# Performance work log

Measured on AMD Instinct MI355X. Metric: run time of the kernel, lower is better.

## Reference

```python
import jax, jax.numpy as jnp
import numpy as np

B, S, E, H = 4, 1024, 512, 8
DK = E // H


def setup_inputs() -> dict:
    key = jax.random.key(0)
    ks = jax.random.split(key, 16)
    s = 1.0 / np.sqrt(E)
    inp = {
        "query": jax.random.normal(ks[0], (B, S, E), dtype=jnp.float32),
        "key": jax.random.normal(ks[1], (B, S, E), dtype=jnp.float32),
        "value": jax.random.normal(ks[2], (B, S, E), dtype=jnp.float32),
        "dist_conv": jax.random.uniform(ks[3], (B, S, S), dtype=jnp.float32),
        "mask": jax.random.randint(ks[4], (B, S, S), 0, 2, dtype=jnp.int32),
        # four Linear(E, E) layers: q, k, v, out (torch: y = x @ W.T + b)
        "Wq": jax.random.normal(ks[5], (E, E), dtype=jnp.float32) * s,
        "bq": jnp.zeros((E,), dtype=jnp.float32),
        "Wk": jax.random.normal(ks[6], (E, E), dtype=jnp.float32) * s,
        "bk": jnp.zeros((E,), dtype=jnp.float32),
        "Wv": jax.random.normal(ks[7], (E, E), dtype=jnp.float32) * s,
        "bv": jnp.zeros((E,), dtype=jnp.float32),
        "Wo": jax.random.normal(ks[8], (E, E), dtype=jnp.float32) * s,
        "bo": jnp.zeros((E,), dtype=jnp.float32),
        # 1x1 Conv2d(1, H) -> ReLU -> 1x1 Conv2d(H, H)
        "cw1": jax.random.normal(ks[9], (H,), dtype=jnp.float32),  # [out_c] (in_c=1, k=1)
        "cb1": jnp.zeros((H,), dtype=jnp.float32),
        "cw2": jax.random.normal(ks[10], (H, H), dtype=jnp.float32) * (1.0 / np.sqrt(H)),
        "cb2": jnp.zeros((H,), dtype=jnp.float32),
    }
    return inp


def reference(query, key, value, dist_conv, mask, Wq, bq, Wk, bk, Wv, bv, Wo, bo, cw1, cb1, cw2, cb2):
    # projections, split into heads: [B, H, S, DK]
    def proj(x, W, b):
        y = jnp.einsum("bse,fe->bsf", x, W) + b
        return y.reshape(B, S, H, DK).transpose(0, 2, 1, 3)

    q = proj(query, Wq, bq)
    k = proj(key, Wk, bk)
    v = proj(value, Wv, bv)

    # 1x1 conv stack on distance matrix: [B,S,S] -> [B,H,S,S]
    t = jax.nn.relu(dist_conv[:, None] * cw1[None, :, None, None] + cb1[None, :, None, None])
    bias = jnp.einsum("bhij,gh->bgij", t, cw2) + cb2[None, :, None, None]

    scores = jnp.einsum("bhqd,bhkd->bhqk", q, k) / jnp.sqrt(jnp.float32(DK))
    scores = scores * bias
    scores = jnp.where(mask[:, None] == 0, jnp.float32(-1e9), scores)
    p_attn = jax.nn.softmax(scores, axis=-1)

    x = jnp.einsum("bhqk,bhkd->bhqd", p_attn, v)
    x = x.transpose(0, 2, 1, 3).reshape(B, S, E)
    return jnp.einsum("bse,fe->bsf", x, Wo) + bo
```

## Files before the change

### kernel.cpp

```cpp
#include <hip/hip_runtime.h>
#include <hip/hip_bf16.h>
#include <math.h>

#define B_ 4
#define S_ 1024
#define E_ 512
#define H_ 8
#define DK_ 64

typedef short bf16x8 __attribute__((ext_vector_type(8)));
typedef float f32x4 __attribute__((ext_vector_type(4)));

#define MFMA16(a, b, c) __builtin_amdgcn_mfma_f32_16x16x32_bf16((a), (b), (c), 0, 0, 0)
#define cfence() asm volatile("" ::: "memory")

__device__ __forceinline__ void gl_lds16(const void* gptr, void* lptr) {
    __builtin_amdgcn_global_load_lds(
        (const __attribute__((address_space(1))) unsigned int*)gptr,
        (__attribute__((address_space(3))) unsigned int*)lptr,
        16, 0, 0);
}

__device__ __forceinline__ unsigned short bf16_bits(float v) {
    __hip_bfloat16 h = __float2bfloat16(v);
    return *(unsigned short*)&h;
}

__global__ __launch_bounds__(256) void prep(
    const float* __restrict__ q, const float* __restrict__ k, const float* __restrict__ v,
    const float* __restrict__ wq, const float* __restrict__ wk,
    const float* __restrict__ wv, const float* __restrict__ wo,
    const float* __restrict__ dist, const int* __restrict__ mask,
    __hip_bfloat16* qc, __hip_bfloat16* kc, __hip_bfloat16* vc,
    __hip_bfloat16* wqc, __hip_bfloat16* wkc, __hip_bfloat16* wvc, __hip_bfloat16* woc,
    __hip_bfloat16* __restrict__ dM) {
    const int blk = blockIdx.x;
    const int tid = threadIdx.x;
    if (blk >= 3584) {
        const int bi = blk - 3584;
        const size_t base = (size_t)bi * 2048 + (size_t)tid * 8;
        float4 d4a = *(const float4*)(dist + base);
        float4 d4b = *(const float4*)(dist + base + 4);
        int4 m4a = *(const int4*)(mask + base);
        int4 m4b = *(const int4*)(mask + base + 4);
        float dv[8] = {d4a.x, d4a.y, d4a.z, d4a.w, d4b.x, d4b.y, d4b.z, d4b.w};
        int mv[8] = {m4a.x, m4a.y, m4a.z, m4a.w, m4b.x, m4b.y, m4b.z, m4b.w};
        union { unsigned short us[8]; uint4 u4; } o;
#pragma unroll
        for (int e = 0; e < 8; ++e) {
            unsigned short u = bf16_bits(dv[e]);
            if (mv[e] == 0) u = 0xFF80u;
            o.us[e] = u;
        }
        *(uint4*)(dM + base) = o.u4;
        return;
    }
    const float* src;
    __hip_bfloat16* dst;
    int base;
    if (blk < 1024)      { src = q; dst = qc; base = blk; }
    else if (blk < 2048) { src = k; dst = kc; base = blk - 1024; }
    else if (blk < 3072) { src = v; dst = vc; base = blk - 2048; }
    else {
        const int wz = (blk - 3072) >> 7;
        base = (blk - 3072) & 127;
        switch (wz) {
            case 0: src = wq; dst = wqc; break;
            case 1: src = wk; dst = wkc; break;
            case 2: src = wv; dst = wvc; break;
            default: src = wo; dst = woc; break;
        }
    }
    const int idx = (base * 256 + tid) * 8;
    float4 a = *(const float4*)(src + idx);
    float4 bb = *(const float4*)(src + idx + 4);
    union { __hip_bfloat16 h[8]; uint4 u; } o;
    o.h[0] = __float2bfloat16(a.x);  o.h[1] = __float2bfloat16(a.y);
    o.h[2] = __float2bfloat16(a.z);  o.h[3] = __float2bfloat16(a.w);
    o.h[4] = __float2bfloat16(bb.x); o.h[5] = __float2bfloat16(bb.y);
    o.h[6] = __float2bfloat16(bb.z); o.h[7] = __float2bfloat16(bb.w);
    *(uint4*)(dst + idx) = o.u;
}

template <int MT, int NROWS_W, int NT>
__device__ __forceinline__ void gemm_core64(const __hip_bfloat16* A, const __hip_bfloat16* W,
                                            char* sA, char* sW, int m0, int n0,
                                            f32x4 acc[MT][NT]) {
    const int t = threadIdx.x;
    const int w = t >> 6, lane = t & 63;
    const int wm = (w >> 1) * (MT * 16), wn = (w & 1) * (NT * 16);
    const int g = lane >> 4, ln = lane & 15;
    const int AB = MT * 4096;
    const int WB = NROWS_W * 128;

    const char* aaddr[MT];
    const char* waddr[NROWS_W / 32];
#pragma unroll
    for (int i = 0; i < MT; ++i) {
        int L = (i * 4 + w) * 64 + lane;
        int r = L >> 3, cs = L & 7;
        int c = cs ^ (r & 7);
        aaddr[i] = (const char*)A + (size_t)(m0 + r) * 1024 + c * 16;
    }
#pragma unroll
    for (int i = 0; i < NROWS_W / 32; ++i) {
        int L = (i * 4 + w) * 64 + lane;
        int r = L >> 3, cs = L & 7;
        int c = cs ^ (r & 7);
        waddr[i] = (const char*)W + (size_t)(n0 + r) * 1024 + c * 16;
    }

#pragma unroll
    for (int i = 0; i < MT; ++i) {
        gl_lds16(aaddr[i], sA + (i * 4 + w) * 1024);
        aaddr[i] += 128;
    }
#pragma unroll
    for (int i = 0; i < NROWS_W / 32; ++i) {
        gl_lds16(waddr[i], sW + (i * 4 + w) * 1024);
        waddr[i] += 128;
    }

    for (int kc = 0; kc < 8; ++kc) {
        const int cur = kc & 1;
        __syncthreads();
        if (kc < 7) {
            char* nA = sA + (cur ^ 1) * AB;
            char* nW = sW + (cur ^ 1) * WB;
#pragma unroll
            for (int i = 0; i < MT; ++i) {
                gl_lds16(aaddr[i], nA + (i * 4 + w) * 1024);
                aaddr[i] += 128;
            }
#pragma unroll
            for (int i = 0; i < NROWS_W / 32; ++i) {
                gl_lds16(waddr[i], nW + (i * 4 + w) * 1024);
                waddr[i] += 128;
            }
        }
        const char* cA = sA + cur * AB;
        const char* cW = sW + cur * WB;
#pragma unroll
        for (int ks = 0; ks < 2; ++ks) {
            bf16x8 af[MT], bf[NT];
#pragma unroll
            for (int mt = 0; mt < MT; ++mt) {
                int m = wm + mt * 16 + ln;
                int c = ks * 4 + g;
                af[mt] = *(const bf16x8*)(cA + m * 128 + (c ^ (m & 7)) * 16);
            }
#pragma unroll
            for (int nt = 0; nt < NT; ++nt) {
                int n = wn + nt * 16 + ln;
                int c = ks * 4 + g;
                bf[nt] = *(const bf16x8*)(cW + n * 128 + (c ^ (n & 7)) * 16);
            }
#pragma unroll
            for (int mt = 0; mt < MT; ++mt)
#pragma unroll
                for (int nt = 0; nt < NT; ++nt)
                    acc[mt][nt] = MFMA16(af[mt], bf[nt], acc[mt][nt]);
        }
    }
}

__global__ __launch_bounds__(256) void proj_gemm(
    const __hip_bfloat16* __restrict__ qc, const __hip_bfloat16* __restrict__ kc,
    const __hip_bfloat16* __restrict__ vc,
    const __hip_bfloat16* __restrict__ wqc, const __hip_bfloat16* __restrict__ wkc,
    const __hip_bfloat16* __restrict__ wvc,
    const float* __restrict__ bq, const float* __restrict__ bk, const float* __restrict__ bv,
    __hip_bfloat16* qbh, __hip_bfloat16* kbh, __hip_bfloat16* vt) {
    __shared__ char smem[49152];
    char* sA = smem;
    char* sW = smem + 32768;
    const int z = blockIdx.z;
    const __hip_bfloat16* A;
    const __hip_bfloat16* W;
    const float* bias;
    __hip_bfloat16* dst;
    float scale;
    if (z == 0)      { A = qc; W = wqc; bias = bq; dst = qbh; scale = 0.125f; }
    else if (z == 1) { A = kc; W = wkc; bias = bk; dst = kbh; scale = 1.f; }
    else             { A = vc; W = wvc; bias = bv; dst = vt;  scale = 1.f; }

    const int m0 = blockIdx.y * 128, n0 = blockIdx.x * 64;
    f32x4 acc[4][2] = {};
    gemm_core64<4, 64, 2>(A, W, sA, sW, m0, n0, acc);
    __syncthreads();

    const int t = threadIdx.x;
    const int w = t >> 6, lane = t & 63;
    const int wm = (w >> 1) * 64, wn = (w & 1) * 32;
    const int g = lane >> 4, ln = lane & 15;
    const int b = m0 >> 10;
    const int h = n0 >> 6;
    float bv2[2];
#pragma unroll
    for (int nt = 0; nt < 2; ++nt) bv2[nt] = bias[n0 + wn + nt * 16 + ln];

    __hip_bfloat16* T = (__hip_bfloat16*)smem;
    if (z != 2) {
#pragma unroll
        for (int mt = 0; mt < 4; ++mt)
#pragma unroll
            for (int nt = 0; nt < 2; ++nt)
#pragma unroll
                for (int r = 0; r < 4; ++r)
                    T[(wm + mt * 16 + g * 4 + r) * 72 + wn + nt * 16 + ln] =
                        __float2bfloat16((acc[mt][nt][r] + bv2[nt]) * scale);
        __syncthreads();
        const int row = t >> 1, sel = t & 1;
        const char* srow = (const char*)T + row * 144 + sel * 64;
        char* gdst = (char*)dst +
                     (((size_t)(b * 8 + h) * 1024 + (m0 & 1023) + row) * 64 + sel * 32) * 2;
#pragma unroll
        for (int j = 0; j < 4; ++j)
            *(uint4*)(gdst + j * 16) = *(const uint4*)(srow + j * 16);
    } else {
#pragma unroll
        for (int mt = 0; mt < 4; ++mt)
#pragma unroll
            for (int nt = 0; nt < 2; ++nt)
#pragma unroll
                for (int r = 0; r < 4; ++r)
                    T[(wm + mt * 16 + g * 4 + r) * 65 + wn + nt * 16 + ln] =
                        __float2bfloat16(acc[mt][nt][r] + bv2[nt]);
        __syncthreads();
        const int dk = t >> 2, qd = t & 3;
        union { __hip_bfloat16 hh[32]; uint4 u[4]; } P;
#pragma unroll
        for (int i = 0; i < 32; ++i)
            P.hh[i] = T[(qd * 32 + i) * 65 + dk];
        char* gdst = (char*)vt +
                     (((size_t)(b * 8 + h) * 64 + dk) * 1024 + (m0 & 1023) + qd * 32) * 2;
#pragma unroll
        for (int j = 0; j < 4; ++j)
            *(uint4*)(gdst + j * 16) = P.u[j];
    }
}

__global__ __launch_bounds__(256) void out_gemm(
    const __hip_bfloat16* __restrict__ X, const __hip_bfloat16* __restrict__ woc,
    const float* __restrict__ bo, float* __restrict__ out) {
    __shared__ char smem[32768];
    char* sA = smem;
    char* sW = smem + 16384;
    const int m0 = blockIdx.y * 64, n0 = blockIdx.x * 64;
    f32x4 acc[2][2] = {};
    gemm_core64<2, 64, 2>(X, woc, sA, sW, m0, n0, acc);

    const int t = threadIdx.x;
    const int w = t >> 6, lane = t & 63;
    const int wm = (w >> 1) * 32, wn = (w & 1) * 32;
    const int g = lane >> 4, ln = lane & 15;
    float bv2[2];
#pragma unroll
    for (int nt = 0; nt < 2; ++nt) bv2[nt] = bo[n0 + wn + nt * 16 + ln];
#pragma unroll
    for (int mt = 0; mt < 2; ++mt)
#pragma unroll
        for (int nt = 0; nt < 2; ++nt)
#pragma unroll
            for (int r = 0; r < 4; ++r) {
                int m = m0 + wm + mt * 16 + g * 4 + r;
                int f = n0 + wn + nt * 16 + ln;
                out[(size_t)m * 512 + f] = acc[mt][nt][r] + bv2[nt];
            }
}

__global__ __launch_bounds__(256) void attn_one(
    const __hip_bfloat16* __restrict__ Qb, const __hip_bfloat16* __restrict__ Kb,
    const __hip_bfloat16* __restrict__ Vt, const __hip_bfloat16* __restrict__ dM,
    const float* __restrict__ cw1, const float* __restrict__ cb1,
    const float* __restrict__ cw2, const float* __restrict__ cb2,
    __hip_bfloat16* __restrict__ X) {
    __shared__ char sK[2][8192];
    __shared__ char sV[2][8192];
    __shared__ __hip_bfloat16 sP[4][16 * 72];

    const int t = threadIdx.x, w = t >> 6, lane = t & 63;
    const int g = lane >> 4, ln = lane & 15;
    const int wg = blockIdx.x;
    const int xcd = wg & 7, sub = wg >> 3;
    const int bh = xcd * 4 + (sub >> 4);
    const int q0 = (sub & 15) * 64;

    char* sp = (char*)sP[w];

    const int gh = bh & 7;
    float Pc = 0.f, Cc = cb2[gh];
#pragma unroll
    for (int h = 0; h < 8; ++h) {
        float w2 = cw2[gh * 8 + h];
        Pc = fmaf(w2, fmaxf(cw1[h], 0.f), Pc);
        Cc = fmaf(w2, fmaxf(cb1[h], 0.f), Cc);
    }
    const float LOG2E = 1.4426950408889634f;
    Pc *= LOG2E; Cc *= LOG2E;

    bf16x8 qf[2];
    {
        const char* qbase = (const char*)Qb + ((size_t)bh * 1024 + q0 + w * 16 + ln) * 128;
        qf[0] = *(const bf16x8*)(qbase + g * 16);
        qf[1] = *(const bf16x8*)(qbase + 64 + g * 16);
    }

    const char* kaddr[2];
    const char* vaddr[2];
#pragma unroll
    for (int i = 0; i < 2; ++i) {
        int L = (i * 4 + w) * 64 + lane;
        int r = L >> 3, cs = L & 7;
        int c = cs ^ (r & 7);
        kaddr[i] = (const char*)Kb + (size_t)bh * 131072 + (size_t)r * 128 + c * 16;
        vaddr[i] = (const char*)Vt + (size_t)bh * 131072 + (size_t)r * 2048 + c * 16;
    }
    const char* daddr = (const char*)dM +
        (((size_t)(bh >> 3) * 1024 + q0 + w * 16 + ln) * 1024 + g * 4) * 2;

    float m_st = -1e30f, l_st = 0.f;
    f32x4 O[4] = {};

#pragma unroll
    for (int i = 0; i < 2; ++i) {
        gl_lds16(kaddr[i], sK[0] + (i * 4 + w) * 1024);
        gl_lds16(vaddr[i], sV[0] + (i * 4 + w) * 1024);
        kaddr[i] += 8192;
        vaddr[i] += 128;
    }
    uint2 dn0 = *(const uint2*)(daddr);
    uint2 dn1 = *(const uint2*)(daddr + 32);
    uint2 dn2 = *(const uint2*)(daddr + 64);
    uint2 dn3 = *(const uint2*)(daddr + 96);
    daddr += 128;

    for (int it = 0; it < 16; ++it) {
        const int cur = it & 1;
        __syncthreads();
        uint2 d0 = dn0, d1 = dn1, d2 = dn2, d3 = dn3;
        if (it < 15) {
#pragma unroll
            for (int i = 0; i < 2; ++i) {
                gl_lds16(kaddr[i], sK[cur ^ 1] + (i * 4 + w) * 1024);
                gl_lds16(vaddr[i], sV[cur ^ 1] + (i * 4 + w) * 1024);
                kaddr[i] += 8192;
                vaddr[i] += 128;
            }
            dn0 = *(const uint2*)(daddr);
            dn1 = *(const uint2*)(daddr + 32);
            dn2 = *(const uint2*)(daddr + 64);
            dn3 = *(const uint2*)(daddr + 96);
            daddr += 128;
        }

        f32x4 scv[4] = {};
#pragma unroll
        for (int tt = 0; tt < 4; ++tt)
#pragma unroll
            for (int ks = 0; ks < 2; ++ks) {
                int key = tt * 16 + ln;
                int cc = ks * 4 + g;
                bf16x8 kf = *(const bf16x8*)(sK[cur] + key * 128 + (cc ^ (key & 7)) * 16);
                scv[tt] = MFMA16(kf, qf[ks], scv[tt]);
            }

        float s2[16];
#pragma unroll
        for (int tt = 0; tt < 4; ++tt) {
            uint2 dd = (tt == 0) ? d0 : (tt == 1) ? d1 : (tt == 2) ? d2 : d3;
            unsigned int bbv[4];
            bbv[0] = dd.x << 16;
            bbv[1] = dd.x & 0xFFFF0000u;
            bbv[2] = dd.y << 16;
            bbv[3] = dd.y & 0xFFFF0000u;
#pragma unroll
            for (int rr = 0; rr < 4; ++rr) {
                float f = fmaf(__uint_as_float(bbv[rr]), Pc, Cc);
                float s = scv[tt][rr] * f;
                s = (bbv[rr] == 0xFF800000u) ? -1e9f : s;
                s2[tt * 4 + rr] = s;
            }
        }
        float t8[8];
#pragma unroll
        for (int j = 0; j < 8; ++j) t8[j] = fmaxf(s2[2 * j], s2[2 * j + 1]);
        float t4a = fmaxf(t8[0], t8[1]), t4b = fmaxf(t8[2], t8[3]);
        float t4c = fmaxf(t8[4], t8[5]), t4d = fmaxf(t8[6], t8[7]);
        float mx = fmaxf(fmaxf(t4a, t4b), fmaxf(t4c, t4d));
        mx = fmaxf(mx, __shfl_xor(mx, 16));
        mx = fmaxf(mx, __shfl_xor(mx, 32));

        const bool full = __any(mx > m_st + 8.f);
        float alpha = 1.f;
        if (full) {
            const float mnew = fmaxf(m_st, mx);
            alpha = __builtin_amdgcn_exp2f(m_st - mnew);
            m_st = mnew;
        }
        float pv16[16];
#pragma unroll
        for (int i = 0; i < 16; ++i) pv16[i] = __builtin_amdgcn_exp2f(s2[i] - m_st);
        float r8[8];
#pragma unroll
        for (int j = 0; j < 8; ++j) r8[j] = pv16[2 * j] + pv16[2 * j + 1];
        float r4a = r8[0] + r8[1], r4b = r8[2] + r8[3];
        float r4c = r8[4] + r8[5], r4d = r8[6] + r8[7];
        float rs = (r4a + r4b) + (r4c + r4d);
        rs += __shfl_xor(rs, 16);
        rs += __shfl_xor(rs, 32);
        l_st = (full ? l_st * alpha : l_st) + rs;

#pragma unroll
        for (int tt = 0; tt < 4; ++tt) {
            union { unsigned short u[4]; uint2 v; } pk;
            pk.u[0] = bf16_bits(pv16[tt * 4 + 0]);
            pk.u[1] = bf16_bits(pv16[tt * 4 + 1]);
            pk.u[2] = bf16_bits(pv16[tt * 4 + 2]);
            pk.u[3] = bf16_bits(pv16[tt * 4 + 3]);
            *(uint2*)(sp + ln * 144 + tt * 32 + g * 8) = pk.v;
        }
        cfence();

        if (full) {
            float al4[4];
#pragma unroll
            for (int rr = 0; rr < 4; ++rr)
                al4[rr] = __shfl(alpha, (lane & 48) + g * 4 + rr);
#pragma unroll
            for (int tt = 0; tt < 4; ++tt)
#pragma unroll
                for (int rr = 0; rr < 4; ++rr) O[tt][rr] *= al4[rr];
        }

#pragma unroll
        for (int ks = 0; ks < 2; ++ks) {
            bf16x8 pf = *(const bf16x8*)(sp + ln * 144 + ks * 64 + g * 16);
#pragma unroll
            for (int tt = 0; tt < 4; ++tt) {
                int dk = tt * 16 + ln;
                int cc = ks * 4 + g;
                bf16x8 vf = *(const bf16x8*)(sV[cur] + dk * 128 + (cc ^ (dk & 7)) * 16);
                O[tt] = MFMA16(pf, vf, O[tt]);
            }
        }
        cfence();
    }

    const float inv = 1.f / l_st;
    float iv4[4];
#pragma unroll
    for (int rr = 0; rr < 4; ++rr)
        iv4[rr] = __shfl(inv, (lane & 48) + g * 4 + rr);
    const int b = bh >> 3, h = bh & 7;
#pragma unroll
    for (int rr = 0; rr < 4; ++rr) {
        const int s = q0 + w * 16 + g * 4 + rr;
        __hip_bfloat16* xrow = X + ((size_t)(b * 1024 + s)) * 512 + h * 64;
#pragma unroll
        for (int tt = 0; tt < 4; ++tt)
            xrow[tt * 16 + ln] = __float2bfloat16(O[tt][rr] * iv4[rr]);
    }
}

extern "C" void kernel_launch(void* const* d_in, const int* in_sizes, int n_in,
                              void* d_out, int out_size, void* d_ws, size_t ws_size,
                              hipStream_t stream) {
    (void)in_sizes; (void)n_in; (void)out_size; (void)ws_size;
    const float* query = (const float*)d_in[0];
    const float* key   = (const float*)d_in[1];
    const float* value = (const float*)d_in[2];
    const float* dist  = (const float*)d_in[3];
    const int*   mask  = (const int*)d_in[4];
    const float* Wq = (const float*)d_in[5];
    const float* bq = (const float*)d_in[6];
    const float* Wk = (const float*)d_in[7];
    const float* bk = (const float*)d_in[8];
    const float* Wv = (const float*)d_in[9];
    const float* bv = (const float*)d_in[10];
    const float* Wo = (const float*)d_in[11];
    const float* bo = (const float*)d_in[12];
    const float* cw1 = (const float*)d_in[13];
    const float* cb1 = (const float*)d_in[14];
    const float* cw2 = (const float*)d_in[15];
    const float* cb2 = (const float*)d_in[16];
    float* out = (float*)d_out;

    char* ws = (char*)d_ws;
    const size_t MB = 1 << 20;
    __hip_bfloat16* qc  = (__hip_bfloat16*)(ws + 0 * MB);
    __hip_bfloat16* kc  = (__hip_bfloat16*)(ws + 4 * MB);
    __hip_bfloat16* vc  = (__hip_bfloat16*)(ws + 8 * MB);
    __hip_bfloat16* wqc = (__hip_bfloat16*)(ws + 12 * MB);
    __hip_bfloat16* wkc = (__hip_bfloat16*)(ws + 12 * MB + 512 * 1024);
    __hip_bfloat16* wvc = (__hip_bfloat16*)(ws + 13 * MB);
    __hip_bfloat16* woc = (__hip_bfloat16*)(ws + 13 * MB + 512 * 1024);
    __hip_bfloat16* qbh = (__hip_bfloat16*)(ws + 14 * MB);
    __hip_bfloat16* kbh = (__hip_bfloat16*)(ws + 18 * MB);
    __hip_bfloat16* vt  = (__hip_bfloat16*)(ws + 22 * MB);
    __hip_bfloat16* x   = (__hip_bfloat16*)(ws + 26 * MB);
    __hip_bfloat16* dMp = (__hip_bfloat16*)(ws + 32 * MB);

    hipLaunchKernelGGL(prep, dim3(5632), dim3(256), 0, stream,
                       query, key, value, Wq, Wk, Wv, Wo, dist, mask,
                       qc, kc, vc, wqc, wkc, wvc, woc, dMp);
    hipLaunchKernelGGL(proj_gemm, dim3(8, 32, 3), dim3(256), 0, stream,
                       qc, kc, vc, wqc, wkc, wvc, bq, bk, bv, qbh, kbh, vt);
    hipLaunchKernelGGL(attn_one, dim3(512), dim3(256), 0, stream,
                       qbh, kbh, vt, dMp, cw1, cb1, cw2, cb2, x);
    hipLaunchKernelGGL(out_gemm, dim3(8, 64), dim3(256), 0, stream,
                       x, woc, bo, out);
}
```

Before: 177.7 us.

## Retile projection GEMM to 64x128 and remap block IDs across XCDs

The projection GEMM changes from 128x64 tiles to 64x128 tiles, so each block covers two heads, and launches on a flattened 1D grid of 768 blocks. The epilogue writes for Q/K and for the transposed V are reworked to match. Both the projection and output GEMMs now use a block-index swizzle ((bid&7)*N + bid>>3), so consecutive tiles land on the same XCD and share L2 locality. The aim is better cache reuse and occupancy, at the cost of more complex indexing and different LDS usage.

```diff
diff --git a/kernel.cpp b/kernel.cpp
--- a/kernel.cpp
+++ b/kernel.cpp
@@ -173,8 +173,15 @@
     __hip_bfloat16* qbh, __hip_bfloat16* kbh, __hip_bfloat16* vt) {
     __shared__ char smem[49152];
     char* sA = smem;
-    char* sW = smem + 32768;
-    const int z = blockIdx.z;
+    char* sW = smem + 16384;
+
+    const int bid = blockIdx.x;
+    const int tile = (bid & 7) * 96 + (bid >> 3);
+    const int z = tile >> 8;
+    const int rem = tile & 255;
+    const int m0 = (rem >> 2) * 64;
+    const int n0 = (rem & 3) * 128;
+
     const __hip_bfloat16* A;
     const __hip_bfloat16* W;
     const float* bias;
@@ -184,56 +191,57 @@
     else if (z == 1) { A = kc; W = wkc; bias = bk; dst = kbh; scale = 1.f; }
     else             { A = vc; W = wvc; bias = bv; dst = vt;  scale = 1.f; }
 
-    const int m0 = blockIdx.y * 128, n0 = blockIdx.x * 64;
-    f32x4 acc[4][2] = {};
-    gemm_core64<4, 64, 2>(A, W, sA, sW, m0, n0, acc);
+    f32x4 acc[2][4] = {};
+    gemm_core64<2, 128, 4>(A, W, sA, sW, m0, n0, acc);
     __syncthreads();
 
     const int t = threadIdx.x;
     const int w = t >> 6, lane = t & 63;
-    const int wm = (w >> 1) * 64, wn = (w & 1) * 32;
+    const int wm = (w >> 1) * 32, wn = (w & 1) * 64;
     const int g = lane >> 4, ln = lane & 15;
     const int b = m0 >> 10;
-    const int h = n0 >> 6;
-    float bv2[2];
-#pragma unroll
-    for (int nt = 0; nt < 2; ++nt) bv2[nt] = bias[n0 + wn + nt * 16 + ln];
+    float bv4[4];
+#pragma unroll
+    for (int nt = 0; nt < 4; ++nt) bv4[nt] = bias[n0 + wn + nt * 16 + ln];
 
     __hip_bfloat16* T = (__hip_bfloat16*)smem;
     if (z != 2) {
 #pragma unroll
-        for (int mt = 0; mt < 4; ++mt)
-#pragma unroll
-            for (int nt = 0; nt < 2; ++nt)
+        for (int mt = 0; mt < 2; ++mt)
+#pragma unroll
+            for (int nt = 0; nt < 4; ++nt)
 #pragma unroll
                 for (int r = 0; r < 4; ++r)
-                    T[(wm + mt * 16 + g * 4 + r) * 72 + wn + nt * 16 + ln] =
-                        __float2bfloat16((acc[mt][nt][r] + bv2[nt]) * scale);
+                    T[(wm + mt * 16 + g * 4 + r) * 136 + wn + nt * 16 + ln] =
+                        __float2bfloat16((acc[mt][nt][r] + bv4[nt]) * scale);
         __syncthreads();
-        const int row = t >> 1, sel = t & 1;
-        const char* srow = (const char*)T + row * 144 + sel * 64;
+        const int row = t >> 2, quarter = t & 3;
+        const char* srow = (const char*)T + row * 272 + quarter * 64;
+        const int s = (m0 & 1023) + row;
+        const int h = (n0 >> 6) + (quarter >> 1);
         char* gdst = (char*)dst +
-                     (((size_t)(b * 8 + h) * 1024 + (m0 & 1023) + row) * 64 + sel * 32) * 2;
+                     (((size_t)(b * 8 + h) * 1024 + s) * 64 + (quarter & 1) * 32) * 2;
 #pragma unroll
         for (int j = 0; j < 4; ++j)
             *(uint4*)(gdst + j * 16) = *(const uint4*)(srow + j * 16);
     } else {
 #pragma unroll
-        for (int mt = 0; mt < 4; ++mt)
-#pragma unroll
-            for (int nt = 0; nt < 2; ++nt)
+        for (int mt = 0; mt < 2; ++mt)
+#pragma unroll
+            for (int nt = 0; nt < 4; ++nt)
 #pragma unroll
                 for (int r = 0; r < 4; ++r)
-                    T[(wm + mt * 16 + g * 4 + r) * 65 + wn + nt * 16 + ln] =
-                        __float2bfloat16(acc[mt][nt][r] + bv2[nt]);
+                    T[(wm + mt * 16 + g * 4 + r) * 129 + wn + nt * 16 + ln] =
+                        __float2bfloat16(acc[mt][nt][r] + bv4[nt]);
         __syncthreads();
-        const int dk = t >> 2, qd = t & 3;
+        const int c = t >> 1, sel = t & 1;
         union { __hip_bfloat16 hh[32]; uint4 u[4]; } P;
 #pragma unroll
         for (int i = 0; i < 32; ++i)
-            P.hh[i] = T[(qd * 32 + i) * 65 + dk];
+            P.hh[i] = T[(sel * 32 + i) * 129 + c];
+        const int h = (n0 >> 6) + (c >> 6), dkk = c & 63;
         char* gdst = (char*)vt +
-                     (((size_t)(b * 8 + h) * 64 + dk) * 1024 + (m0 & 1023) + qd * 32) * 2;
+                     (((size_t)(b * 8 + h) * 64 + dkk) * 1024 + (m0 & 1023) + sel * 32) * 2;
 #pragma unroll
         for (int j = 0; j < 4; ++j)
             *(uint4*)(gdst + j * 16) = P.u[j];
@@ -246,7 +254,12 @@
     __shared__ char smem[32768];
     char* sA = smem;
     char* sW = smem + 16384;
-    const int m0 = blockIdx.y * 64, n0 = blockIdx.x * 64;
+
+    const int bid = blockIdx.x;
+    const int tile = (bid & 7) * 64 + (bid >> 3);
+    const int m0 = (tile >> 3) * 64;
+    const int n0 = (tile & 7) * 64;
+
     f32x4 acc[2][2] = {};
     gemm_core64<2, 64, 2>(X, woc, sA, sW, m0, n0, acc);
 
@@ -504,10 +517,10 @@
     hipLaunchKernelGGL(prep, dim3(5632), dim3(256), 0, stream,
                        query, key, value, Wq, Wk, Wv, Wo, dist, mask,
                        qc, kc, vc, wqc, wkc, wvc, woc, dMp);
-    hipLaunchKernelGGL(proj_gemm, dim3(8, 32, 3), dim3(256), 0, stream,
+    hipLaunchKernelGGL(proj_gemm, dim3(768), dim3(256), 0, stream,
                        qc, kc, vc, wqc, wkc, wvc, bq, bk, bv, qbh, kbh, vt);
     hipLaunchKernelGGL(attn_one, dim3(512), dim3(256), 0, stream,
                        qbh, kbh, vt, dMp, cw1, cb1, cw2, cb2, x);
-    hipLaunchKernelGGL(out_gemm, dim3(8, 64), dim3(256), 0, stream,
+    hipLaunchKernelGGL(out_gemm, dim3(512), dim3(256), 0, stream,
                        x, woc, bo, out);
 }
```

Result: faster. 172.0 us (-3.2%).
